# Kernel optimization log

Measured on AMD Instinct MI355X. Metric: run time of the kernel, lower is better.

The kernel has to match this reference:

```python
import jax, jax.numpy as jnp
import numpy as np

N_NODES = 10000
N_EDGES = 640000
D_IN = 128
D_OUT = 128


def setup_inputs() -> dict:
    key = jax.random.key(0)
    k_x, k_val, k_w, k_row, k_col = jax.random.split(key, 5)
    # Glorot init for weight, zeros for bias (matches _weight_init)
    limit = float(np.sqrt(6.0 / (D_IN + D_OUT)))
    weight = jax.random.uniform(k_w, (D_IN, D_OUT), jnp.float32, -limit, limit)
    return {
        "x": jax.random.normal(k_x, (N_NODES, D_IN), jnp.float32),
        "adj_val": jax.random.uniform(k_val, (N_EDGES,), jnp.float32),  # normalized edge weights of sparse adj
        "weight": weight,
        "bias": jnp.zeros((D_OUT,), jnp.float32),
        "adj_row": jax.random.randint(k_row, (N_EDGES,), 0, N_NODES, jnp.int32),
        "adj_col": jax.random.randint(k_col, (N_EDGES,), 0, N_NODES, jnp.int32),
    }


def reference(x, adj_val, weight, bias, adj_row, adj_col):
    # dense GEMM: h = x @ W  -> [N, D_OUT]
    h = jnp.matmul(x, weight)
    # SpMM with COO adjacency: out[r] = sum_{e: row[e]=r} val[e] * h[col[e]]
    msg = adj_val[:, None] * h[adj_col]  # [E, D_OUT] gather + scale
    out = jax.ops.segment_sum(msg, adj_row, num_segments=x.shape[0])
    return out + bias
```

## Files before the change

kernel.cpp:

```cpp
#include <hip/hip_runtime.h>

#define N_NODES 10000
#define N_EDGES 640000
#define D 128

#define GEMM_BLOCKS 157
#define TOT_BLOCKS 256
#define CAP 32
#define OVF_CAP 8192
#define LSTR 136
#define QPAD 272

typedef unsigned int uint32;
typedef unsigned short u16;
using short8 = __attribute__((ext_vector_type(8))) short;
using f32x4  = __attribute__((ext_vector_type(4))) float;

__device__ __forceinline__ uint32 f2bf_bits(float f) {
    uint32 u = __float_as_uint(f);
    return (u + 0x7FFFu + ((u >> 16) & 1u)) >> 16;
}
__device__ __forceinline__ uint32 pack2(float lo, float hi) {
    return f2bf_bits(lo) | (f2bf_bits(hi) << 16);
}

__device__ __forceinline__ void scat_one(int r, uint32 rc, int s,
                                         int* __restrict__ cursor,
                                         uint32* __restrict__ region,
                                         int* ovf_cnt, uint2* ovf)
{
    int pos = atomicAdd(&cursor[s * N_NODES + r], 1);
    if (pos < CAP) {
        region[(r * 8 + s) * CAP + pos] = rc;
    } else {
        int o = atomicAdd(ovf_cnt, 1);
        if (o < OVF_CAP) ovf[o] = make_uint2((uint32)r, rc);
    }
}

__global__ __launch_bounds__(256) void gemm_scatter_kernel(
    const float* __restrict__ x, const float* __restrict__ w,
    const int* __restrict__ row, const int* __restrict__ col,
    const float* __restrict__ val,
    uint32* __restrict__ h2, int* __restrict__ cursor,
    int* __restrict__ ovf_cnt, uint2* __restrict__ ovf,
    uint32* __restrict__ region)
{
    const int t = threadIdx.x;

    if (blockIdx.x < GEMM_BLOCKS) {
        __shared__ u16 Xs[64 * LSTR];
        __shared__ u16 Ws[128 * LSTR];

        #pragma unroll
        for (int i = 0; i < 8; ++i) {
            int lin = t + i * 256;
            int rw  = lin >> 5;
            int f4  = lin & 31;
            int gr = blockIdx.x * 64 + rw;
            if (gr >= N_NODES) gr = N_NODES - 1;
            float4 xv = *(const float4*)&x[(size_t)gr * D + f4 * 4];
            *(uint2*)&Xs[rw * LSTR + f4 * 4] =
                make_uint2(pack2(xv.x, xv.y), pack2(xv.z, xv.w));
        }
        #pragma unroll
        for (int i = 0; i < 32; ++i) {
            int lin = t + i * 256;
            int c = lin & 127;
            int m = lin >> 7;
            float w0 = w[(2 * m) * D + c];
            float w1 = w[(2 * m + 1) * D + c];
            *(uint32*)&Ws[c * LSTR + 2 * m] = pack2(w0, w1);
        }
        __syncthreads();

        const int wv = t >> 6, lane = t & 63;
        const int q = lane >> 4, cl = lane & 15;
        f32x4 acc[8] = {};
        const u16* arow = &Xs[(wv * 16 + cl) * LSTR];
        #pragma unroll
        for (int k0 = 0; k0 < D; k0 += 32) {
            short8 af = *(const short8*)&arow[k0 + q * 8];
            #pragma unroll
            for (int ct = 0; ct < 8; ++ct) {
                short8 bf = *(const short8*)&Ws[(ct * 16 + cl) * LSTR + k0 + q * 8];
                acc[ct] = __builtin_amdgcn_mfma_f32_16x16x32_bf16(af, bf, acc[ct], 0, 0, 0);
            }
        }
        #pragma unroll
        for (int reg = 0; reg < 4; ++reg) {
            int node = blockIdx.x * 64 + wv * 16 + q * 4 + reg;
            if (node < N_NODES) {
                uint32* base = h2 + (size_t)node * 64 + cl;
                #pragma unroll
                for (int ct = 0; ct < 4; ++ct)
                    base[ct * 16] = pack2(acc[ct][reg], acc[ct + 4][reg]);
            }
        }
    }

    {
        const int xcc = blockIdx.x & 7;
        const int tid    = blockIdx.x * 256 + t;
        const int stride = TOT_BLOCKS * 256;
        const int4*   row4 = (const int4*)row;
        const int4*   col4 = (const int4*)col;
        const float4* val4 = (const float4*)val;
        for (int i = tid; i < N_EDGES / 4; i += stride) {
            int4 r = row4[i]; int4 c = col4[i]; float4 v = val4[i];
            scat_one(r.x, (uint32)c.x | (f2bf_bits(v.x) << 16), xcc, cursor, region, ovf_cnt, ovf);
            scat_one(r.y, (uint32)c.y | (f2bf_bits(v.y) << 16), xcc, cursor, region, ovf_cnt, ovf);
            scat_one(r.z, (uint32)c.z | (f2bf_bits(v.z) << 16), xcc, cursor, region, ovf_cnt, ovf);
            scat_one(r.w, (uint32)c.w | (f2bf_bits(v.w) << 16), xcc, cursor, region, ovf_cnt, ovf);
        }
    }
}

__global__ __launch_bounds__(256) void spmm_kernel(
    const uint32* __restrict__ region, const int* __restrict__ cursor,
    const int* __restrict__ ovf_cnt, const uint2* __restrict__ ovf,
    const uint32* __restrict__ h2, const float* __restrict__ bias,
    float* __restrict__ out)
{
    __shared__ uint32 qbuf[4 * QPAD];
    const int t = threadIdx.x;
    const int lane = t & 63;
    const int wid  = t >> 6;
    const int r = blockIdx.x * 4 + wid;
    uint32* qb = &qbuf[wid * QPAD];

    uint32 rl[4];
    #pragma unroll
    for (int i = 0; i < 4; ++i)
        rl[i] = region[r * 256 + i * 64 + lane];

    int ns[8], pref[9];
    pref[0] = 0;
    #pragma unroll
    for (int s = 0; s < 8; ++s) {
        int c = cursor[s * N_NODES + r];
        ns[s] = (c < CAP) ? c : CAP;
        pref[s + 1] = pref[s] + ns[s];
    }
    const int ntot = pref[8];

    #pragma unroll
    for (int i = 0; i < 4; ++i) {
        int p  = lane & 31;
        int hi = lane >> 5;
        int n_  = hi ? ns[2 * i + 1]   : ns[2 * i];
        int pf  = hi ? pref[2 * i + 1] : pref[2 * i];
        if (p < n_) qb[pf + p] = rl[i];
    }
    if (lane < 16) qb[ntot + lane] = 0;
    __builtin_amdgcn_s_waitcnt(0);

    const int npad = (ntot + 7) & ~7;
    float a0 = 0.f, a1 = 0.f;

    uint32 rq0,rq1,rq2,rq3,rq4,rq5,rq6,rq7;
    uint32 hh0,hh1,hh2,hh3,hh4,hh5,hh6,hh7;
    rq0 = qb[0]; hh0 = h2[((rq0 & 0xFFFFu) << 6) + lane];
    rq1 = qb[1]; hh1 = h2[((rq1 & 0xFFFFu) << 6) + lane];
    rq2 = qb[2]; hh2 = h2[((rq2 & 0xFFFFu) << 6) + lane];
    rq3 = qb[3]; hh3 = h2[((rq3 & 0xFFFFu) << 6) + lane];
    rq4 = qb[4]; hh4 = h2[((rq4 & 0xFFFFu) << 6) + lane];
    rq5 = qb[5]; hh5 = h2[((rq5 & 0xFFFFu) << 6) + lane];
    rq6 = qb[6]; hh6 = h2[((rq6 & 0xFFFFu) << 6) + lane];
    rq7 = qb[7]; hh7 = h2[((rq7 & 0xFFFFu) << 6) + lane];

#define CONSUME_PREFETCH(RQ, HH, P)                                          \
    {                                                                        \
        a0 = fmaf(__uint_as_float(RQ & 0xFFFF0000u),                         \
                  __uint_as_float(HH << 16), a0);                            \
        a1 = fmaf(__uint_as_float(RQ & 0xFFFF0000u),                         \
                  __uint_as_float(HH & 0xFFFF0000u), a1);                    \
        uint32 rn = qb[j + 8 + P];                                           \
        RQ = rn; HH = h2[((rn & 0xFFFFu) << 6) + lane];                      \
    }

    for (int j = 0; j < npad; j += 8) {
        CONSUME_PREFETCH(rq0, hh0, 0)
        CONSUME_PREFETCH(rq1, hh1, 1)
        CONSUME_PREFETCH(rq2, hh2, 2)
        CONSUME_PREFETCH(rq3, hh3, 3)
        CONSUME_PREFETCH(rq4, hh4, 4)
        CONSUME_PREFETCH(rq5, hh5, 5)
        CONSUME_PREFETCH(rq6, hh6, 6)
        CONSUME_PREFETCH(rq7, hh7, 7)
    }
#undef CONSUME_PREFETCH

    int novf = ovf_cnt[0];
    if (novf > OVF_CAP) novf = OVF_CAP;
    for (int k = 0; k < novf; ++k) {
        uint2 e = ovf[k];
        if (e.x == (uint32)r) {
            uint32 qq = e.y;
            uint32 hv = h2[((qq & 0xFFFFu) << 6) + lane];
            a0 = fmaf(__uint_as_float(qq & 0xFFFF0000u), __uint_as_float(hv << 16), a0);
            a1 = fmaf(__uint_as_float(qq & 0xFFFF0000u), __uint_as_float(hv & 0xFFFF0000u), a1);
        }
    }

    out[(size_t)r * D + lane]      = a0 + bias[lane];
    out[(size_t)r * D + 64 + lane] = a1 + bias[lane + 64];
}

extern "C" void kernel_launch(void* const* d_in, const int* in_sizes, int n_in,
                              void* d_out, int out_size, void* d_ws, size_t ws_size,
                              hipStream_t stream)
{
    const float* x    = (const float*)d_in[0];
    const float* aval = (const float*)d_in[1];
    const float* w    = (const float*)d_in[2];
    const float* bias = (const float*)d_in[3];
    const int* arow   = (const int*)d_in[4];
    const int* acol   = (const int*)d_in[5];

    char* ws = (char*)d_ws;
    uint32* h2     = (uint32*)(ws);
    int*    cursor = (int*)(ws + 2560000);
    int*    ovfcnt = (int*)(ws + 2880000);
    uint2*  ovf    = (uint2*)(ws + 2880064);
    uint32* region = (uint32*)(ws + 2945600);

    hipMemsetAsync(ws + 2560000, 0, 320004, stream);

    gemm_scatter_kernel<<<TOT_BLOCKS, 256, 0, stream>>>(
        x, w, arow, acol, aval, h2, cursor, ovfcnt, ovf, region);
    spmm_kernel<<<N_NODES / 4, 256, 0, stream>>>(
        region, cursor, ovfcnt, ovf, h2, bias, (float*)d_out);
}
```

Baseline: 115.6 us.

## Fuse GEMM, scatter and SpMM into one persistent kernel with grid barrier

Merges the GEMM+scatter kernel and the SpMM kernel into a single persistent launch of 1024 blocks separated by a global atomic spin barrier. GEMM and scatter blocks are split into disjoint roles, with more blocks given to scatter. X rows are loaded straight into registers and packed to bf16, so the X shared tile goes away. The W tile's shared buffer is reused as the SpMM queue. This removes one kernel launch and its tail, but the barrier depends on all 1024 blocks being co-resident, and the SpMM phase now has fewer blocks looping over rows.

```diff
diff --git a/kernel.cpp b/kernel.cpp
--- a/kernel.cpp
+++ b/kernel.cpp
@@ -4,8 +4,9 @@
 #define N_EDGES 640000
 #define D 128
 
+#define GRID 1024
 #define GEMM_BLOCKS 157
-#define TOT_BLOCKS 256
+#define SCAT_BLOCKS (GRID - GEMM_BLOCKS)
 #define CAP 32
 #define OVF_CAP 8192
 #define LSTR 136
@@ -38,31 +39,24 @@
     }
 }
 
-__global__ __launch_bounds__(256) void gemm_scatter_kernel(
+__global__ __launch_bounds__(256, 4) void fused_kernel(
     const float* __restrict__ x, const float* __restrict__ w,
     const int* __restrict__ row, const int* __restrict__ col,
     const float* __restrict__ val,
     uint32* __restrict__ h2, int* __restrict__ cursor,
     int* __restrict__ ovf_cnt, uint2* __restrict__ ovf,
-    uint32* __restrict__ region)
+    uint32* __restrict__ region,
+    const float* __restrict__ bias, float* __restrict__ out,
+    int* __restrict__ bar)
 {
+    __shared__ __align__(16) u16 Ws[128 * LSTR];
     const int t = threadIdx.x;
+    const int lane = t & 63;
+    const int wid  = t >> 6;
 
     if (blockIdx.x < GEMM_BLOCKS) {
-        __shared__ u16 Xs[64 * LSTR];
-        __shared__ u16 Ws[128 * LSTR];
-
-        #pragma unroll
-        for (int i = 0; i < 8; ++i) {
-            int lin = t + i * 256;
-            int rw  = lin >> 5;
-            int f4  = lin & 31;
-            int gr = blockIdx.x * 64 + rw;
-            if (gr >= N_NODES) gr = N_NODES - 1;
-            float4 xv = *(const float4*)&x[(size_t)gr * D + f4 * 4];
-            *(uint2*)&Xs[rw * LSTR + f4 * 4] =
-                make_uint2(pack2(xv.x, xv.y), pack2(xv.z, xv.w));
-        }
+        const int q = lane >> 4, cl = lane & 15;
+
         #pragma unroll
         for (int i = 0; i < 32; ++i) {
             int lin = t + i * 256;
@@ -72,24 +66,34 @@
             float w1 = w[(2 * m + 1) * D + c];
             *(uint32*)&Ws[c * LSTR + 2 * m] = pack2(w0, w1);
         }
+
+        int gr = blockIdx.x * 64 + wid * 16 + cl;
+        if (gr >= N_NODES) gr = N_NODES - 1;
+        const float* xrow = &x[(size_t)gr * D];
+        float4 xv[8];
+        #pragma unroll
+        for (int kk = 0; kk < 4; ++kk) {
+            xv[2 * kk]     = *(const float4*)&xrow[kk * 32 + q * 8];
+            xv[2 * kk + 1] = *(const float4*)&xrow[kk * 32 + q * 8 + 4];
+        }
         __syncthreads();
 
-        const int wv = t >> 6, lane = t & 63;
-        const int q = lane >> 4, cl = lane & 15;
         f32x4 acc[8] = {};
-        const u16* arow = &Xs[(wv * 16 + cl) * LSTR];
-        #pragma unroll
-        for (int k0 = 0; k0 < D; k0 += 32) {
-            short8 af = *(const short8*)&arow[k0 + q * 8];
+        #pragma unroll
+        for (int kk = 0; kk < 4; ++kk) {
+            union { short8 s; uint32 u[4]; } af;
+            float4 a = xv[2 * kk], b = xv[2 * kk + 1];
+            af.u[0] = pack2(a.x, a.y); af.u[1] = pack2(a.z, a.w);
+            af.u[2] = pack2(b.x, b.y); af.u[3] = pack2(b.z, b.w);
             #pragma unroll
             for (int ct = 0; ct < 8; ++ct) {
-                short8 bf = *(const short8*)&Ws[(ct * 16 + cl) * LSTR + k0 + q * 8];
-                acc[ct] = __builtin_amdgcn_mfma_f32_16x16x32_bf16(af, bf, acc[ct], 0, 0, 0);
+                short8 bf = *(const short8*)&Ws[(ct * 16 + cl) * LSTR + kk * 32 + q * 8];
+                acc[ct] = __builtin_amdgcn_mfma_f32_16x16x32_bf16(af.s, bf, acc[ct], 0, 0, 0);
             }
         }
         #pragma unroll
         for (int reg = 0; reg < 4; ++reg) {
-            int node = blockIdx.x * 64 + wv * 16 + q * 4 + reg;
+            int node = blockIdx.x * 64 + wid * 16 + q * 4 + reg;
             if (node < N_NODES) {
                 uint32* base = h2 + (size_t)node * 64 + cl;
                 #pragma unroll
@@ -97,12 +101,10 @@
                     base[ct * 16] = pack2(acc[ct][reg], acc[ct + 4][reg]);
             }
         }
-    }
-
-    {
+    } else {
         const int xcc = blockIdx.x & 7;
-        const int tid    = blockIdx.x * 256 + t;
-        const int stride = TOT_BLOCKS * 256;
+        const int tid    = (blockIdx.x - GEMM_BLOCKS) * 256 + t;
+        const int stride = SCAT_BLOCKS * 256;
         const int4*   row4 = (const int4*)row;
         const int4*   col4 = (const int4*)col;
         const float4* val4 = (const float4*)val;
@@ -114,60 +116,63 @@
             scat_one(r.w, (uint32)c.w | (f2bf_bits(v.w) << 16), xcc, cursor, region, ovf_cnt, ovf);
         }
     }
-}
-
-__global__ __launch_bounds__(256) void spmm_kernel(
-    const uint32* __restrict__ region, const int* __restrict__ cursor,
-    const int* __restrict__ ovf_cnt, const uint2* __restrict__ ovf,
-    const uint32* __restrict__ h2, const float* __restrict__ bias,
-    float* __restrict__ out)
-{
-    __shared__ uint32 qbuf[4 * QPAD];
-    const int t = threadIdx.x;
-    const int lane = t & 63;
-    const int wid  = t >> 6;
-    const int r = blockIdx.x * 4 + wid;
-    uint32* qb = &qbuf[wid * QPAD];
-
-    uint32 rl[4];
-    #pragma unroll
-    for (int i = 0; i < 4; ++i)
-        rl[i] = region[r * 256 + i * 64 + lane];
-
-    int ns[8], pref[9];
-    pref[0] = 0;
-    #pragma unroll
-    for (int s = 0; s < 8; ++s) {
-        int c = cursor[s * N_NODES + r];
-        ns[s] = (c < CAP) ? c : CAP;
-        pref[s + 1] = pref[s] + ns[s];
-    }
-    const int ntot = pref[8];
-
-    #pragma unroll
-    for (int i = 0; i < 4; ++i) {
-        int p  = lane & 31;
-        int hi = lane >> 5;
-        int n_  = hi ? ns[2 * i + 1]   : ns[2 * i];
-        int pf  = hi ? pref[2 * i + 1] : pref[2 * i];
-        if (p < n_) qb[pf + p] = rl[i];
-    }
-    if (lane < 16) qb[ntot + lane] = 0;
-    __builtin_amdgcn_s_waitcnt(0);
-
-    const int npad = (ntot + 7) & ~7;
-    float a0 = 0.f, a1 = 0.f;
-
-    uint32 rq0,rq1,rq2,rq3,rq4,rq5,rq6,rq7;
-    uint32 hh0,hh1,hh2,hh3,hh4,hh5,hh6,hh7;
-    rq0 = qb[0]; hh0 = h2[((rq0 & 0xFFFFu) << 6) + lane];
-    rq1 = qb[1]; hh1 = h2[((rq1 & 0xFFFFu) << 6) + lane];
-    rq2 = qb[2]; hh2 = h2[((rq2 & 0xFFFFu) << 6) + lane];
-    rq3 = qb[3]; hh3 = h2[((rq3 & 0xFFFFu) << 6) + lane];
-    rq4 = qb[4]; hh4 = h2[((rq4 & 0xFFFFu) << 6) + lane];
-    rq5 = qb[5]; hh5 = h2[((rq5 & 0xFFFFu) << 6) + lane];
-    rq6 = qb[6]; hh6 = h2[((rq6 & 0xFFFFu) << 6) + lane];
-    rq7 = qb[7]; hh7 = h2[((rq7 & 0xFFFFu) << 6) + lane];
+
+    __syncthreads();
+    if (t == 0) {
+        __threadfence();
+        __hip_atomic_fetch_add(bar, 1, __ATOMIC_RELAXED, __HIP_MEMORY_SCOPE_AGENT);
+        while (__hip_atomic_load(bar, __ATOMIC_RELAXED, __HIP_MEMORY_SCOPE_AGENT) < GRID)
+            __builtin_amdgcn_s_sleep(2);
+        __threadfence();
+    }
+    __syncthreads();
+
+    {
+        uint32* qbuf = (uint32*)Ws;
+        uint32* qb = &qbuf[wid * QPAD];
+
+        for (int r = blockIdx.x * 4 + wid; r < N_NODES; r += GRID * 4) {
+            __builtin_amdgcn_s_waitcnt(0);
+
+            uint32 rl[4];
+            #pragma unroll
+            for (int i = 0; i < 4; ++i)
+                rl[i] = region[r * 256 + i * 64 + lane];
+
+            int ns[8], pref[9];
+            pref[0] = 0;
+            #pragma unroll
+            for (int s = 0; s < 8; ++s) {
+                int c = cursor[s * N_NODES + r];
+                ns[s] = (c < CAP) ? c : CAP;
+                pref[s + 1] = pref[s] + ns[s];
+            }
+            const int ntot = pref[8];
+
+            #pragma unroll
+            for (int i = 0; i < 4; ++i) {
+                int p  = lane & 31;
+                int hi = lane >> 5;
+                int n_  = hi ? ns[2 * i + 1]   : ns[2 * i];
+                int pf  = hi ? pref[2 * i + 1] : pref[2 * i];
+                if (p < n_) qb[pf + p] = rl[i];
+            }
+            if (lane < 16) qb[ntot + lane] = 0;
+            __builtin_amdgcn_s_waitcnt(0);
+
+            const int npad = (ntot + 7) & ~7;
+            float a0 = 0.f, a1 = 0.f;
+
+            uint32 rq0,rq1,rq2,rq3,rq4,rq5,rq6,rq7;
+            uint32 hh0,hh1,hh2,hh3,hh4,hh5,hh6,hh7;
+            rq0 = qb[0]; hh0 = h2[((rq0 & 0xFFFFu) << 6) + lane];
+            rq1 = qb[1]; hh1 = h2[((rq1 & 0xFFFFu) << 6) + lane];
+            rq2 = qb[2]; hh2 = h2[((rq2 & 0xFFFFu) << 6) + lane];
+            rq3 = qb[3]; hh3 = h2[((rq3 & 0xFFFFu) << 6) + lane];
+            rq4 = qb[4]; hh4 = h2[((rq4 & 0xFFFFu) << 6) + lane];
+            rq5 = qb[5]; hh5 = h2[((rq5 & 0xFFFFu) << 6) + lane];
+            rq6 = qb[6]; hh6 = h2[((rq6 & 0xFFFFu) << 6) + lane];
+            rq7 = qb[7]; hh7 = h2[((rq7 & 0xFFFFu) << 6) + lane];
 
 #define CONSUME_PREFETCH(RQ, HH, P)                                          \
     {                                                                        \
@@ -179,32 +184,34 @@
         RQ = rn; HH = h2[((rn & 0xFFFFu) << 6) + lane];                      \
     }
 
-    for (int j = 0; j < npad; j += 8) {
-        CONSUME_PREFETCH(rq0, hh0, 0)
-        CONSUME_PREFETCH(rq1, hh1, 1)
-        CONSUME_PREFETCH(rq2, hh2, 2)
-        CONSUME_PREFETCH(rq3, hh3, 3)
-        CONSUME_PREFETCH(rq4, hh4, 4)
-        CONSUME_PREFETCH(rq5, hh5, 5)
-        CONSUME_PREFETCH(rq6, hh6, 6)
-        CONSUME_PREFETCH(rq7, hh7, 7)
-    }
+            for (int j = 0; j < npad; j += 8) {
+                CONSUME_PREFETCH(rq0, hh0, 0)
+                CONSUME_PREFETCH(rq1, hh1, 1)
+                CONSUME_PREFETCH(rq2, hh2, 2)
+                CONSUME_PREFETCH(rq3, hh3, 3)
+                CONSUME_PREFETCH(rq4, hh4, 4)
+                CONSUME_PREFETCH(rq5, hh5, 5)
+                CONSUME_PREFETCH(rq6, hh6, 6)
+                CONSUME_PREFETCH(rq7, hh7, 7)
+            }
 #undef CONSUME_PREFETCH
 
-    int novf = ovf_cnt[0];
-    if (novf > OVF_CAP) novf = OVF_CAP;
-    for (int k = 0; k < novf; ++k) {
-        uint2 e = ovf[k];
-        if (e.x == (uint32)r) {
-            uint32 qq = e.y;
-            uint32 hv = h2[((qq & 0xFFFFu) << 6) + lane];
-            a0 = fmaf(__uint_as_float(qq & 0xFFFF0000u), __uint_as_float(hv << 16), a0);
-            a1 = fmaf(__uint_as_float(qq & 0xFFFF0000u), __uint_as_float(hv & 0xFFFF0000u), a1);
-        }
-    }
-
-    out[(size_t)r * D + lane]      = a0 + bias[lane];
-    out[(size_t)r * D + 64 + lane] = a1 + bias[lane + 64];
+            int novf = ovf_cnt[0];
+            if (novf > OVF_CAP) novf = OVF_CAP;
+            for (int k = 0; k < novf; ++k) {
+                uint2 e = ovf[k];
+                if (e.x == (uint32)r) {
+                    uint32 qq = e.y;
+                    uint32 hv = h2[((qq & 0xFFFFu) << 6) + lane];
+                    a0 = fmaf(__uint_as_float(qq & 0xFFFF0000u), __uint_as_float(hv << 16), a0);
+                    a1 = fmaf(__uint_as_float(qq & 0xFFFF0000u), __uint_as_float(hv & 0xFFFF0000u), a1);
+                }
+            }
+
+            out[(size_t)r * D + lane]      = a0 + bias[lane];
+            out[(size_t)r * D + 64 + lane] = a1 + bias[lane + 64];
+        }
+    }
 }
 
 extern "C" void kernel_launch(void* const* d_in, const int* in_sizes, int n_in,
@@ -222,13 +229,13 @@
     uint32* h2     = (uint32*)(ws);
     int*    cursor = (int*)(ws + 2560000);
     int*    ovfcnt = (int*)(ws + 2880000);
+    int*    bar    = (int*)(ws + 2880004);
     uint2*  ovf    = (uint2*)(ws + 2880064);
     uint32* region = (uint32*)(ws + 2945600);
 
-    hipMemsetAsync(ws + 2560000, 0, 320004, stream);
-
-    gemm_scatter_kernel<<<TOT_BLOCKS, 256, 0, stream>>>(
-        x, w, arow, acol, aval, h2, cursor, ovfcnt, ovf, region);
-    spmm_kernel<<<N_NODES / 4, 256, 0, stream>>>(
-        region, cursor, ovfcnt, ovf, h2, bias, (float*)d_out);
-}
+    hipMemsetAsync(ws + 2560000, 0, 320008, stream);
+
+    fused_kernel<<<GRID, 256, 0, stream>>>(
+        x, w, arow, acol, aval, h2, cursor, ovfcnt, ovf, region,
+        bias, (float*)d_out, bar);
+}
```

Result: slower. 238.8 us (+106.6%).
